# Kernel optimization log

Measured on AMD Instinct MI355X. Metric: run time of the kernel, lower is better.

## Reference

```python
import jax, jax.numpy as jnp
import numpy as np

D_MODEL = 768
HEADS = 12
D_HEAD = D_MODEL // HEADS
D_DYNA = 768
EPS = 1e-5
B, SP, SI = 16, 256, 1024


def _layernorm(x, g, b):
    mu = jnp.mean(x, axis=-1, keepdims=True)
    var = jnp.var(x, axis=-1, keepdims=True)
    return (x - mu) * jax.lax.rsqrt(var + EPS) * g + b


def _mha(q, k, v, wq, bq, wk, bk, wv, bv, wo, bo):
    # weights stored [d_in, d_out]; torch Linear math y = x @ W^T + b is
    # equivalent with transposed storage.
    B_ = q.shape[0]
    qh = (q @ wq + bq).reshape(B_, -1, HEADS, D_HEAD)
    kh = (k @ wk + bk).reshape(B_, -1, HEADS, D_HEAD)
    vh = (v @ wv + bv).reshape(B_, -1, HEADS, D_HEAD)
    scores = jnp.einsum('bqhd,bkhd->bhqk', qh, kh) / np.sqrt(D_HEAD).astype(np.float32)
    attn = jax.nn.softmax(scores, axis=-1)  # dropout disabled (eval)
    out = jnp.einsum('bhqk,bkhd->bqhd', attn, vh).reshape(B_, -1, D_MODEL)
    return out @ wo + bo


def setup_inputs() -> dict:
    key = jax.random.key(0)
    ks = iter(jax.random.split(key, 40))
    s = 0.02
    d = {
        'image': jax.random.normal(next(ks), (B, SI, D_MODEL), jnp.float32),
        'prompt': jax.random.normal(next(ks), (B, SP, D_MODEL), jnp.float32),
        'posi': jax.random.normal(next(ks), (B, SI, D_MODEL), jnp.float32),
        'posp': jax.random.normal(next(ks), (B, SP, D_MODEL), jnp.float32),
    }
    for ln in ('ln_p1', 'ln_p2', 'ln_p3', 'ln_i1'):
        d[ln + '_g'] = jnp.ones((D_MODEL,), jnp.float32)
        d[ln + '_b'] = jnp.zeros((D_MODEL,), jnp.float32)
    for pre in ('pp', 'pi'):
        for nm in ('q', 'k', 'v', 'o'):
            d[f'{pre}_w{nm}'] = s * jax.random.normal(next(ks), (D_MODEL, D_MODEL), jnp.float32)
            d[f'{pre}_b{nm}'] = jnp.zeros((D_MODEL,), jnp.float32)
    d['ff_w1'] = s * jax.random.normal(next(ks), (D_MODEL, D_MODEL), jnp.float32)
    d['ff_b1'] = jnp.zeros((D_MODEL,), jnp.float32)
    d['ff_w2'] = s * jax.random.normal(next(ks), (D_MODEL, D_DYNA), jnp.float32)
    d['ff_b2'] = jnp.zeros((D_DYNA,), jnp.float32)
    return d


def reference(image, prompt, posi, posp,
              ln_p1_g, ln_p1_b, ln_p2_g, ln_p2_b, ln_p3_g, ln_p3_b, ln_i1_g, ln_i1_b,
              pp_wq, pp_bq, pp_wk, pp_bk, pp_wv, pp_bv, pp_wo, pp_bo,
              pi_wq, pi_bq, pi_wk, pi_bk, pi_wv, pi_bv, pi_wo, pi_bo,
              ff_w1, ff_b1, ff_w2, ff_b2):
    prompt0 = prompt + posp
    xp = _layernorm(prompt0, ln_p1_g, ln_p1_b)
    xp = _mha(xp, xp, xp, pp_wq, pp_bq, pp_wk, pp_bk, pp_wv, pp_bv, pp_wo, pp_bo)
    prompt = prompt + xp  # dropout_p1 is identity in eval
    xp = _layernorm(prompt + prompt0, ln_p2_g, ln_p2_b)
    xi = _layernorm(image + posi, ln_i1_g, ln_i1_b)
    xp = _mha(xp, xi, xi, pi_wq, pi_bq, pi_wk, pi_bk, pi_wv, pi_bv, pi_wo, pi_bo)
    prompt = prompt + xp  # dropout_p2 identity
    xp = _layernorm(prompt + prompt0, ln_p3_g, ln_p3_b)
    xp = jax.nn.relu(xp @ ff_w1 + ff_b1) @ ff_w2 + ff_b2
    return xp
```

## Files before the change

kernel.cpp:

```cpp
#include <hip/hip_runtime.h>
#include <hip/hip_bf16.h>
#include <stdint.h>
#include <math.h>

#define D_MODEL 768
#define HEADS 12
#define D_HEAD 64
#define BATCH 16
#define SP 256
#define SI 1024
#define NP (BATCH * SP)
#define NI (BATCH * SI)

#define GLOBAL_AS __attribute__((address_space(1)))
#define LDS_AS    __attribute__((address_space(3)))

typedef __attribute__((ext_vector_type(8))) short  frag_ab;
typedef __attribute__((ext_vector_type(4))) float  frag_cd;

static __device__ __forceinline__ ushort f2bf(float f) {
  __hip_bfloat16 h = __float2bfloat16(f);
  return *(ushort*)&h;
}
static __device__ __forceinline__ float bf2f(ushort u) {
  return __bfloat162float(*(__hip_bfloat16*)&u);
}
static __device__ __forceinline__ bool probe_bf(const uint32_t* p) {
  return p[0] == 0x3F803F80u;
}

struct Prep {
  const void* wsrc[10]; ushort* wdst[10];
  const void* vsrc[18]; float* vdst;
};

__global__ __launch_bounds__(256) void prep_kernel(Prep p, const uint32_t* probe) {
  const bool isbf = probe_bf(probe);
  const int z = blockIdx.z;
  if (z < 10) {
    __shared__ float tile[32][33];
    const int tx = threadIdx.x & 31, ty = threadIdx.x >> 5;
    const int x0 = blockIdx.x * 32, y0 = blockIdx.y * 32;
    const void* src = p.wsrc[z];
    ushort* dst = p.wdst[z];
#pragma unroll
    for (int i = 0; i < 4; i++) {
      const int y = y0 + ty + i * 8;
      float v;
      if (isbf) v = bf2f(((const ushort*)src)[(size_t)y * 768 + x0 + tx]);
      else      v = ((const float*)src)[(size_t)y * 768 + x0 + tx];
      tile[ty + i * 8][tx] = v;
    }
    __syncthreads();
#pragma unroll
    for (int i = 0; i < 4; i++) {
      const int row = x0 + ty + i * 8;
      const int col = y0 + tx;
      dst[(size_t)row * 768 + col] = f2bf(tile[tx][ty + i * 8]);
    }
  } else {
    const int idx = (blockIdx.y * 24 + blockIdx.x) * 256 + threadIdx.x;
    if (idx < 18 * 768) {
      const int e = idx / 768, i = idx - e * 768;
      float v;
      if (isbf) v = bf2f(((const ushort*)p.vsrc[e])[i]);
      else      v = ((const float*)p.vsrc[e])[i];
      p.vdst[idx] = v;
    }
  }
}

struct LNJob {
  const void* a; const void* b;
  const float* g; const float* be;
  float* sum_out; ushort* ln_out;
  int nrows; int abf;
};

__global__ __launch_bounds__(192) void add_ln2(LNJob J0, LNJob J1, const uint32_t* probe) {
  int row = blockIdx.x;
  LNJob j = (row < J0.nrows) ? J0 : J1;
  if (row >= J0.nrows) row -= J0.nrows;
  const int tid = threadIdx.x;
  const size_t base = (size_t)row * D_MODEL;
  const int c0 = tid * 4;
  const bool isbf = j.abf && probe_bf(probe);
  float x[4];
  if (isbf) {
    const uint2 ua = *(const uint2*)((const ushort*)j.a + base + c0);
    const uint2 ub = *(const uint2*)((const ushort*)j.b + base + c0);
    const ushort* pa = (const ushort*)&ua;
    const ushort* pb = (const ushort*)&ub;
#pragma unroll
    for (int t = 0; t < 4; t++) x[t] = bf2f(pa[t]) + bf2f(pb[t]);
  } else {
    const float4 fa = *(const float4*)((const float*)j.a + base + c0);
    const float4 fb = *(const float4*)((const float*)j.b + base + c0);
    x[0] = fa.x + fb.x; x[1] = fa.y + fb.y; x[2] = fa.z + fb.z; x[3] = fa.w + fb.w;
  }
  if (j.sum_out) {
    float4 s4; s4.x = x[0]; s4.y = x[1]; s4.z = x[2]; s4.w = x[3];
    *(float4*)&j.sum_out[base + c0] = s4;
  }
  __shared__ float rs[192], rq[192];
  __shared__ float stats[2];
  rs[tid] = x[0] + x[1] + x[2] + x[3];
  rq[tid] = x[0]*x[0] + x[1]*x[1] + x[2]*x[2] + x[3]*x[3];
  __syncthreads();
  if (tid < 64) {
    float s = rs[tid] + rs[tid + 64] + rs[tid + 128];
    float q = rq[tid] + rq[tid + 64] + rq[tid + 128];
#pragma unroll
    for (int o = 32; o > 0; o >>= 1) { s += __shfl_down(s, o); q += __shfl_down(q, o); }
    if (tid == 0) {
      const float mu  = s * (1.0f / D_MODEL);
      const float var = q * (1.0f / D_MODEL) - mu * mu;
      stats[0] = mu;
      stats[1] = rsqrtf(var + 1e-5f);
    }
  }
  __syncthreads();
  const float mu = stats[0], inv = stats[1];
  const float4 gv = *(const float4*)&j.g[c0];
  const float4 bv = *(const float4*)&j.be[c0];
  uint2 ou;
  ushort* oe = (ushort*)&ou;
  oe[0] = f2bf((x[0] - mu) * inv * gv.x + bv.x);
  oe[1] = f2bf((x[1] - mu) * inv * gv.y + bv.y);
  oe[2] = f2bf((x[2] - mu) * inv * gv.z + bv.z);
  oe[3] = f2bf((x[3] - mu) * inv * gv.w + bv.w);
  *(uint2*)(j.ln_out + base + c0) = ou;
}

template<int BM>
__global__ __launch_bounds__(256) void gemm_k(
    const ushort* __restrict__ A, const ushort* __restrict__ Bt,
    const float* __restrict__ bias,
    const void* __restrict__ resid, int rmode,
    void* __restrict__ C, int relu, int omode,
    const uint32_t* __restrict__ probe, int X) {
  __shared__ ushort As[BM * 32];
  __shared__ ushort Bs[128 * 32];
  const int tid  = threadIdx.x;
  const int lane = tid & 63, w = tid >> 6;
  const int wr = w >> 1, wc = w & 1;
  const int ml = lane & 15, kq = lane >> 4;
  const int bid = blockIdx.x;
  const int rest = bid >> 3;
  const int x = rest % X, y = (bid & 7) + 8 * (rest / X);
  const int m0 = y * BM, n0 = x * 128;
  constexpr int MT   = BM / 32;
  constexpr int ASEG = BM / 16;
  constexpr int NSEG = (ASEG + 8) / 4;

  frag_cd acc[MT][4] = {};

  for (int k0 = 0; k0 < 768; k0 += 32) {
#pragma unroll
    for (int i = 0; i < NSEG; i++) {
      const int s = w + i * 4;
      const bool isA = (s < ASEG);
      const int seg = isA ? s : (s - ASEG);
      const int r   = seg * 16 + (lane >> 2);
      const int kof = k0 + (lane & 3) * 8;
      if (isA)
        __builtin_amdgcn_global_load_lds((const GLOBAL_AS void*)(A + (size_t)(m0 + r) * 768 + kof),
            (LDS_AS void*)((LDS_AS ushort*)As + seg * 512), 16, 0, 0);
      else
        __builtin_amdgcn_global_load_lds((const GLOBAL_AS void*)(Bt + (size_t)(n0 + r) * 768 + kof),
            (LDS_AS void*)((LDS_AS ushort*)Bs + seg * 512), 16, 0, 0);
    }
    __syncthreads();

    frag_ab af[MT], bf4[4];
#pragma unroll
    for (int t = 0; t < MT; t++)
      af[t] = *(const frag_ab*)&As[(wr * (BM / 2) + t * 16 + ml) * 32 + kq * 8];
#pragma unroll
    for (int t = 0; t < 4; t++)
      bf4[t] = *(const frag_ab*)&Bs[(wc * 64 + t * 16 + ml) * 32 + kq * 8];
#pragma unroll
    for (int mt = 0; mt < MT; mt++)
#pragma unroll
      for (int nt = 0; nt < 4; nt++)
        acc[mt][nt] = __builtin_amdgcn_mfma_f32_16x16x32_bf16(
            af[mt], bf4[nt], acc[mt][nt], 0, 0, 0);
    __syncthreads();
  }

  const bool obf = (omode == 1) || (omode == 2 && probe_bf(probe));
  const bool rbf = (rmode == 2) && probe_bf(probe);
#pragma unroll
  for (int mt = 0; mt < MT; mt++) {
#pragma unroll
    for (int nt = 0; nt < 4; nt++) {
      const int row0 = m0 + wr * (BM / 2) + mt * 16 + kq * 4;
      const int col  = n0 + wc * 64 + nt * 16 + ml;
      const float bc = bias[col];
#pragma unroll
      for (int r = 0; r < 4; r++) {
        const size_t off = (size_t)(row0 + r) * 768 + col;
        float v = acc[mt][nt][r] + bc;
        if (rmode != 0)
          v += rbf ? bf2f(((const ushort*)resid)[off]) : ((const float*)resid)[off];
        if (relu) v = fmaxf(v, 0.f);
        if (obf) ((ushort*)C)[off] = f2bf(v);
        else     ((float*)C)[off]  = v;
      }
    }
  }
}

struct GJob {
  const ushort* A; const ushort* Bt; const float* bias;
  ushort* o0; ushort* o1; ushort* vT;
  int X; int vsub; int shift;
};

#define BAR   __builtin_amdgcn_s_barrier()
#define LGKM0 do { asm volatile("s_waitcnt lgkmcnt(0)" ::: "memory"); \
                   __builtin_amdgcn_sched_barrier(0); } while (0)
#define VMC4  do { asm volatile("s_waitcnt vmcnt(4)" ::: "memory"); \
                   __builtin_amdgcn_sched_barrier(0); } while (0)

#define RD_A(SL) do { \
  const ushort* _b = &lds[SL][0][0]; \
  _Pragma("unroll") for (int _m = 0; _m < 4; ++_m) \
  _Pragma("unroll") for (int _k = 0; _k < 2; ++_k) \
    aF[_m][_k] = *(const frag_ab*)(_b + ((wr << 6) + _m * 16 + ml) * 64 + \
                                   (((_k << 5) + (kq << 3)) ^ swz)); \
} while (0)

#define RD_B(DST, SL, no) do { \
  const ushort* _b = &lds[SL][1][0]; \
  _Pragma("unroll") for (int _n = 0; _n < 2; ++_n) \
  _Pragma("unroll") for (int _k = 0; _k < 2; ++_k) \
    DST[_n][_k] = *(const frag_ab*)(_b + ((wc << 6) + (no) + _n * 16 + ml) * 64 + \
                                    (((_k << 5) + (kq << 3)) ^ swz)); \
} while (0)

#define MM(NB, BF) do { \
  __builtin_amdgcn_s_setprio(1); \
  _Pragma("unroll") for (int _m = 0; _m < 4; ++_m) \
  _Pragma("unroll") for (int _n = 0; _n < 2; ++_n) \
  _Pragma("unroll") for (int _k = 0; _k < 2; ++_k) \
    acc[_m][(NB) + _n] = __builtin_amdgcn_mfma_f32_16x16x32_bf16( \
        aF[_m][_k], BF[_n][_k], acc[_m][(NB) + _n], 0, 0, 0); \
  __builtin_amdgcn_s_setprio(0); \
} while (0)

#define STAGE(SL, RG, PTR, RBASE, KT) do { \
  const ushort* _p = (PTR) + (size_t)((RBASE) + srow) * 768 + ((KT) << 6) + scol; \
  _Pragma("unroll") for (int _j = 0; _j < 4; ++_j) \
    __builtin_amdgcn_global_load_lds( \
        (const GLOBAL_AS void*)(_p + (size_t)(_j * 32) * 768), \
        (LDS_AS void*)((LDS_AS ushort*)&lds[SL][RG][0] + (((_j << 2) + w) << 9)), \
        16, 0, 0); \
} while (0)

__global__ __launch_bounds__(256, 2) void gemm_mega128(GJob J0, GJob J1, int n0blocks) {
  __shared__ __align__(16) ushort lds[2][2][8192];
  int bid = blockIdx.x;
  GJob j = (bid < n0blocks) ? J0 : J1;
  if (bid >= n0blocks) bid -= n0blocks;
  const int tid  = threadIdx.x;
  const int lane = tid & 63, w = tid >> 6;
  const int wr = w >> 1, wc = w & 1;
  const int ml = lane & 15, kq = lane >> 4;
  const int rest = bid >> 3;
  const int x = rest % j.X, y = (bid & 7) + 8 * (rest / j.X);
  const int m0 = y << 7, n0 = x << 7;
  const int srow = (w << 3) + (lane >> 3);
  const int scol = (((lane & 7) ^ (lane >> 3)) << 3);
  const int swz  = (ml & 7) << 3;
  const ushort* jA = j.A;
  const ushort* jB = j.Bt;

  frag_cd acc[4][4] = {};
  frag_ab aF[4][2], bF0[2][2], bF1[2][2];

  STAGE(0, 0, jA, m0, 0);
  STAGE(0, 1, jB, n0, 0);
  STAGE(1, 0, jA, m0, 1);
  VMC4;
  BAR;

  for (int it = 0; it < 6; ++it) {
    const int t1  = 2 * it + 1;
    const int tn0 = (2 * it + 2 < 12) ? 2 * it + 2 : 11;
    const int tn1 = (2 * it + 3 < 12) ? 2 * it + 3 : 11;
    RD_A(0); RD_B(bF0, 0, 0);
    STAGE(1, 1, jB, n0, t1);
    BAR; LGKM0;
    MM(0, bF0);
    BAR;
    RD_B(bF1, 0, 32);
    STAGE(0, 0, jA, m0, tn0);
    BAR; LGKM0;
    MM(2, bF1);
    VMC4;
    BAR;
    RD_A(1); RD_B(bF0, 1, 0);
    STAGE(0, 1, jB, n0, tn0);
    BAR; LGKM0;
    MM(0, bF0);
    BAR;
    RD_B(bF1, 1, 32);
    STAGE(1, 0, jA, m0, tn1);
    BAR; LGKM0;
    MM(2, bF1);
    VMC4;
    BAR;
  }

  const int sub  = x / 6;
  const int mask = (1 << j.shift) - 1;
#pragma unroll
  for (int mt = 0; mt < 4; mt++) {
#pragma unroll
    for (int nt = 0; nt < 4; nt++) {
      const int row0 = m0 + wr * 64 + mt * 16 + kq * 4;
      const int col  = n0 + wc * 64 + nt * 16 + ml;
      const float bc = j.bias[col];
      if (sub == j.vsub) {
        const int hcol = col - sub * 768;
        const int hh = hcol >> 6, dd = hcol & 63;
        const int bb = row0 >> j.shift;
        const int jj = row0 & mask;
        uint2 pack;
        ushort* pe = (ushort*)&pack;
#pragma unroll
        for (int r = 0; r < 4; r++) pe[r] = f2bf(acc[mt][nt][r] + bc);
        *(uint2*)(j.vT + ((((size_t)(bb * HEADS + hh) << 6) + dd) << j.shift) + jj) = pack;
      } else {
        ushort* out = (sub == 0) ? j.o0 : j.o1;
        const int cl = col - sub * 768;
#pragma unroll
        for (int r = 0; r < 4; r++)
          out[(size_t)(row0 + r) * 768 + cl] = f2bf(acc[mt][nt][r] + bc);
      }
    }
  }
}

#undef RD_A
#undef RD_B
#undef MM
#undef STAGE

#define FS 68
__global__ __launch_bounds__(256) void fattn_mfma(
    const ushort* __restrict__ Q, const ushort* __restrict__ Kp,
    const ushort* __restrict__ vT, ushort* __restrict__ O, int Skv) {
  __shared__ __align__(16) ushort Qs[64 * FS];
  __shared__ __align__(16) ushort Ks[64 * FS];
  __shared__ __align__(16) ushort Vt[64 * FS];
  __shared__ __align__(16) ushort Ps[64 * FS];
  const int tid  = threadIdx.x;
  const int lane = tid & 63, w = tid >> 6;
  const int ml   = lane & 15, kq = lane >> 4;
  const int bid = blockIdx.x;
  const int g8  = bid & 7;
  const int qt  = (bid >> 3) & 3;
  const int g   = (bid >> 5) * 8 + g8;
  const int h   = g % HEADS;
  const int b   = g / HEADS;
  const int q0  = qt * 64;
  const ushort* Qb  = Q  + ((size_t)b * SP + q0) * D_MODEL + h * D_HEAD;
  const ushort* Kb  = Kp + (size_t)b * Skv * D_MODEL + h * D_HEAD;
  const ushort* vTb = vT + (size_t)g * 64 * Skv;

  for (int c = tid; c < 512; c += 256) {
    const int r = c >> 3, p = c & 7;
    *(uint4*)&Qs[r * FS + p * 8] = *(const uint4*)(Qb + (size_t)r * D_MODEL + p * 8);
  }
  __syncthreads();
  frag_ab qa[2];
#pragma unroll
  for (int kc = 0; kc < 2; kc++)
    qa[kc] = *(const frag_ab*)&Qs[(w * 16 + ml) * FS + kc * 32 + kq * 8];

  frag_cd oc[4] = {};
  float m_i[4], l_i[4];
#pragma unroll
  for (int r = 0; r < 4; r++) { m_i[r] = -1e30f; l_i[r] = 0.f; }
  const float SCL = 0.125f * 1.44269504f;

  for (int j0 = 0; j0 < Skv; j0 += 64) {
    __syncthreads();
    for (int c = tid; c < 512; c += 256) {
      const int r = c >> 3, p = c & 7;
      *(uint4*)&Ks[r * FS + p * 8] = *(const uint4*)(Kb + (size_t)(j0 + r) * D_MODEL + p * 8);
      *(uint4*)&Vt[r * FS + p * 8] = *(const uint4*)(vTb + (size_t)r * Skv + j0 + p * 8);
    }
    __syncthreads();

    frag_cd sc[4] = {};
#pragma unroll
    for (int nt = 0; nt < 4; nt++)
#pragma unroll
      for (int kc = 0; kc < 2; kc++) {
        const frag_ab bfr = *(const frag_ab*)&Ks[(nt * 16 + ml) * FS + kc * 32 + kq * 8];
        sc[nt] = __builtin_amdgcn_mfma_f32_16x16x32_bf16(qa[kc], bfr, sc[nt], 0, 0, 0);
      }
#pragma unroll
    for (int nt = 0; nt < 4; nt++)
#pragma unroll
      for (int r = 0; r < 4; r++) sc[nt][r] *= SCL;

    float al[4];
#pragma unroll
    for (int r = 0; r < 4; r++) {
      float mx = fmaxf(fmaxf(sc[0][r], sc[1][r]), fmaxf(sc[2][r], sc[3][r]));
#pragma unroll
      for (int m = 1; m < 16; m <<= 1) mx = fmaxf(mx, __shfl_xor(mx, m, 16));
      const float mnew = fmaxf(m_i[r], mx);
      al[r] = exp2f(m_i[r] - mnew);
      float p[4], s = 0.f;
#pragma unroll
      for (int nt = 0; nt < 4; nt++) { p[nt] = exp2f(sc[nt][r] - mnew); s += p[nt]; }
#pragma unroll
      for (int m = 1; m < 16; m <<= 1) s += __shfl_xor(s, m, 16);
      l_i[r] = l_i[r] * al[r] + s;
      m_i[r] = mnew;
      const int prow = (w * 16 + kq * 4 + r) * FS;
#pragma unroll
      for (int nt = 0; nt < 4; nt++) Ps[prow + nt * 16 + ml] = f2bf(p[nt]);
    }
#pragma unroll
    for (int dt = 0; dt < 4; dt++)
#pragma unroll
      for (int r = 0; r < 4; r++) oc[dt][r] *= al[r];

#pragma unroll
    for (int kc = 0; kc < 2; kc++) {
      const frag_ab pa = *(const frag_ab*)&Ps[(w * 16 + ml) * FS + kc * 32 + kq * 8];
#pragma unroll
      for (int dt = 0; dt < 4; dt++) {
        const frag_ab vb = *(const frag_ab*)&Vt[(dt * 16 + ml) * FS + kc * 32 + kq * 8];
        oc[dt] = __builtin_amdgcn_mfma_f32_16x16x32_bf16(pa, vb, oc[dt], 0, 0, 0);
      }
    }
  }

  float inv[4];
#pragma unroll
  for (int r = 0; r < 4; r++) inv[r] = 1.0f / l_i[r];
#pragma unroll
  for (int dt = 0; dt < 4; dt++)
#pragma unroll
    for (int r = 0; r < 4; r++)
      O[((size_t)b * SP + q0 + w * 16 + kq * 4 + r) * D_MODEL + h * D_HEAD + dt * 16 + ml] =
          f2bf(oc[dt][r] * inv[r]);
}

extern "C" void kernel_launch(void* const* d_in, const int* in_sizes, int n_in,
                              void* d_out, int out_size, void* d_ws, size_t ws_size,
                              hipStream_t stream) {
  (void)in_sizes; (void)n_in; (void)out_size;
  char* base = (char*)d_ws;
  size_t off = 256;
  auto alloc = [&](size_t bytes) -> char* {
    char* p = base + off;
    off = (off + bytes + 255) & ~(size_t)255;
    return p;
  };
  const size_t WB = (size_t)768 * 768 * 2;
  ushort* Wt[10];
  for (int i = 0; i < 10; i++) Wt[i] = (ushort*)alloc(WB);
  float* vecs = (float*)alloc(18 * 768 * 4);
  float* biasF[10];
  for (int i = 0; i < 10; i++) biasF[i] = vecs + i * 768;
  float* lnF = vecs + 10 * 768;
  float* prompt0 = (float*)alloc((size_t)NP * 768 * 4);
  float* cur     = (float*)alloc((size_t)NP * 768 * 4);
  ushort* q_bf   = (ushort*)alloc((size_t)NP * 768 * 2);
  ushort* k_s    = (ushort*)alloc((size_t)NP * 768 * 2);
  ushort* k_c    = (ushort*)alloc((size_t)NI * 768 * 2);
  ushort* xln_bf = (ushort*)alloc((size_t)NP * 768 * 2);
  ushort* xi_bf  = (ushort*)alloc((size_t)NI * 768 * 2);
  ushort* obuf_bf = (ushort*)alloc((size_t)NP * 768 * 2);
  ushort* ffn1_bf = (ushort*)alloc((size_t)NP * 768 * 2);
  ushort* vT_s   = (ushort*)alloc((size_t)BATCH * HEADS * 64 * SP * 2);
  ushort* vT_c   = (ushort*)alloc((size_t)BATCH * HEADS * 64 * SI * 2);
  if (ws_size < off) return;

  const uint32_t* probe = (const uint32_t*)d_in[4];
  const int widx[10] = {12, 14, 16, 18, 20, 22, 24, 26, 28, 30};
  const int bidx[10] = {13, 15, 17, 19, 21, 23, 25, 27, 29, 31};

  Prep pr{};
  for (int i = 0; i < 10; i++) { pr.wsrc[i] = d_in[widx[i]]; pr.wdst[i] = Wt[i]; }
  for (int i = 0; i < 10; i++) pr.vsrc[i] = d_in[bidx[i]];
  for (int i = 0; i < 8;  i++) pr.vsrc[10 + i] = d_in[4 + i];
  pr.vdst = vecs;
  prep_kernel<<<dim3(24, 24, 11), 256, 0, stream>>>(pr, probe);

  float* G1 = lnF + 0 * 768, *B1 = lnF + 1 * 768;
  float* G2 = lnF + 2 * 768, *B2 = lnF + 3 * 768;
  float* G3 = lnF + 4 * 768, *B3 = lnF + 5 * 768;
  float* Gi = lnF + 6 * 768, *Bi = lnF + 7 * 768;

  LNJob L0{d_in[1], d_in[3], G1, B1, prompt0, xln_bf, NP, 1};
  LNJob Li{d_in[0], d_in[2], Gi, Bi, nullptr, xi_bf,  NI, 1};
  add_ln2<<<NP + NI, 192, 0, stream>>>(L0, Li, probe);

  GJob js{xln_bf, Wt[0], biasF[0], q_bf, k_s, vT_s, 18, 2, 8};
  GJob jc{xi_bf,  Wt[5], biasF[5], k_c,  nullptr, vT_c, 12, 1, 10};
  gemm_mega128<<<576 + 1536, 256, 0, stream>>>(js, jc, 576);

  fattn_mfma<<<BATCH * HEADS * (SP / 64), 256, 0, stream>>>(q_bf, k_s, vT_s, obuf_bf, SP);

  gemm_k<64><<<6 * 64, 256, 0, stream>>>(obuf_bf, Wt[3], biasF[3],
      d_in[1], 2, cur, 0, 0, probe, 6);

  LNJob L2{cur, prompt0, G2, B2, nullptr, xln_bf, NP, 0};
  LNJob Lz{}; Lz.nrows = 0;
  add_ln2<<<NP, 192, 0, stream>>>(L2, Lz, probe);

  gemm_k<64><<<6 * 64, 256, 0, stream>>>(xln_bf, Wt[4], biasF[4],
      nullptr, 0, q_bf, 0, 1, probe, 6);

  fattn_mfma<<<BATCH * HEADS * (SP / 64), 256, 0, stream>>>(q_bf, k_c, vT_c, obuf_bf, SI);

  gemm_k<64><<<6 * 64, 256, 0, stream>>>(obuf_bf, Wt[7], biasF[7],
      cur, 1, cur, 0, 0, probe, 6);

  LNJob L3{cur, prompt0, G3, B3, nullptr, xln_bf, NP, 0};
  add_ln2<<<NP, 192, 0, stream>>>(L3, Lz, probe);

  gemm_k<64><<<6 * 64, 256, 0, stream>>>(xln_bf, Wt[8], biasF[8],
      nullptr, 0, ffn1_bf, 1, 1, probe, 6);

  gemm_k<64><<<6 * 64, 256, 0, stream>>>(ffn1_bf, Wt[9], biasF[9],
      nullptr, 0, d_out, 0, 2, probe, 6);
}
```

Measured before the change: 503.9 us.

## Use pipelined 128x128 GEMM for prompt GEMMs and prefetch K/V in attention

Replaces the simple BM=64 GEMM used for the five prompt-side projections with a new kernel built on the swizzled, double-buffered 128x128 engine already used by the fused QKV GEMM, factored into a shared macro. Flash attention now prefetches the next K/V tile into registers while computing on the current one. The goal is better MFMA utilisation and hidden global-load latency. The trade-off is fewer blocks for the 4096-row GEMMs (192 instead of 384), which may underfill the GPU's CUs.

```diff
diff --git a/kernel.cpp b/kernel.cpp
--- a/kernel.cpp
+++ b/kernel.cpp
@@ -132,91 +132,6 @@
   *(uint2*)(j.ln_out + base + c0) = ou;
 }
 
-template<int BM>
-__global__ __launch_bounds__(256) void gemm_k(
-    const ushort* __restrict__ A, const ushort* __restrict__ Bt,
-    const float* __restrict__ bias,
-    const void* __restrict__ resid, int rmode,
-    void* __restrict__ C, int relu, int omode,
-    const uint32_t* __restrict__ probe, int X) {
-  __shared__ ushort As[BM * 32];
-  __shared__ ushort Bs[128 * 32];
-  const int tid  = threadIdx.x;
-  const int lane = tid & 63, w = tid >> 6;
-  const int wr = w >> 1, wc = w & 1;
-  const int ml = lane & 15, kq = lane >> 4;
-  const int bid = blockIdx.x;
-  const int rest = bid >> 3;
-  const int x = rest % X, y = (bid & 7) + 8 * (rest / X);
-  const int m0 = y * BM, n0 = x * 128;
-  constexpr int MT   = BM / 32;
-  constexpr int ASEG = BM / 16;
-  constexpr int NSEG = (ASEG + 8) / 4;
-
-  frag_cd acc[MT][4] = {};
-
-  for (int k0 = 0; k0 < 768; k0 += 32) {
-#pragma unroll
-    for (int i = 0; i < NSEG; i++) {
-      const int s = w + i * 4;
-      const bool isA = (s < ASEG);
-      const int seg = isA ? s : (s - ASEG);
-      const int r   = seg * 16 + (lane >> 2);
-      const int kof = k0 + (lane & 3) * 8;
-      if (isA)
-        __builtin_amdgcn_global_load_lds((const GLOBAL_AS void*)(A + (size_t)(m0 + r) * 768 + kof),
-            (LDS_AS void*)((LDS_AS ushort*)As + seg * 512), 16, 0, 0);
-      else
-        __builtin_amdgcn_global_load_lds((const GLOBAL_AS void*)(Bt + (size_t)(n0 + r) * 768 + kof),
-            (LDS_AS void*)((LDS_AS ushort*)Bs + seg * 512), 16, 0, 0);
-    }
-    __syncthreads();
-
-    frag_ab af[MT], bf4[4];
-#pragma unroll
-    for (int t = 0; t < MT; t++)
-      af[t] = *(const frag_ab*)&As[(wr * (BM / 2) + t * 16 + ml) * 32 + kq * 8];
-#pragma unroll
-    for (int t = 0; t < 4; t++)
-      bf4[t] = *(const frag_ab*)&Bs[(wc * 64 + t * 16 + ml) * 32 + kq * 8];
-#pragma unroll
-    for (int mt = 0; mt < MT; mt++)
-#pragma unroll
-      for (int nt = 0; nt < 4; nt++)
-        acc[mt][nt] = __builtin_amdgcn_mfma_f32_16x16x32_bf16(
-            af[mt], bf4[nt], acc[mt][nt], 0, 0, 0);
-    __syncthreads();
-  }
-
-  const bool obf = (omode == 1) || (omode == 2 && probe_bf(probe));
-  const bool rbf = (rmode == 2) && probe_bf(probe);
-#pragma unroll
-  for (int mt = 0; mt < MT; mt++) {
-#pragma unroll
-    for (int nt = 0; nt < 4; nt++) {
-      const int row0 = m0 + wr * (BM / 2) + mt * 16 + kq * 4;
-      const int col  = n0 + wc * 64 + nt * 16 + ml;
-      const float bc = bias[col];
-#pragma unroll
-      for (int r = 0; r < 4; r++) {
-        const size_t off = (size_t)(row0 + r) * 768 + col;
-        float v = acc[mt][nt][r] + bc;
-        if (rmode != 0)
-          v += rbf ? bf2f(((const ushort*)resid)[off]) : ((const float*)resid)[off];
-        if (relu) v = fmaxf(v, 0.f);
-        if (obf) ((ushort*)C)[off] = f2bf(v);
-        else     ((float*)C)[off]  = v;
-      }
-    }
-  }
-}
-
-struct GJob {
-  const ushort* A; const ushort* Bt; const float* bias;
-  ushort* o0; ushort* o1; ushort* vT;
-  int X; int vsub; int shift;
-};
-
 #define BAR   __builtin_amdgcn_s_barrier()
 #define LGKM0 do { asm volatile("s_waitcnt lgkmcnt(0)" ::: "memory"); \
                    __builtin_amdgcn_sched_barrier(0); } while (0)
@@ -257,6 +172,44 @@
         (LDS_AS void*)((LDS_AS ushort*)&lds[SL][RG][0] + (((_j << 2) + w) << 9)), \
         16, 0, 0); \
 } while (0)
+
+#define ENGINE128() do { \
+  STAGE(0, 0, jA, m0, 0); \
+  STAGE(0, 1, jB, n0, 0); \
+  STAGE(1, 0, jA, m0, 1); \
+  VMC4; BAR; \
+  for (int it = 0; it < 6; ++it) { \
+    const int t1  = 2 * it + 1; \
+    const int tn0 = (2 * it + 2 < 12) ? 2 * it + 2 : 11; \
+    const int tn1 = (2 * it + 3 < 12) ? 2 * it + 3 : 11; \
+    RD_A(0); RD_B(bF0, 0, 0); \
+    STAGE(1, 1, jB, n0, t1); \
+    BAR; LGKM0; \
+    MM(0, bF0); \
+    BAR; \
+    RD_B(bF1, 0, 32); \
+    STAGE(0, 0, jA, m0, tn0); \
+    BAR; LGKM0; \
+    MM(2, bF1); \
+    VMC4; BAR; \
+    RD_A(1); RD_B(bF0, 1, 0); \
+    STAGE(0, 1, jB, n0, tn0); \
+    BAR; LGKM0; \
+    MM(0, bF0); \
+    BAR; \
+    RD_B(bF1, 1, 32); \
+    STAGE(1, 0, jA, m0, tn1); \
+    BAR; LGKM0; \
+    MM(2, bF1); \
+    VMC4; BAR; \
+  } \
+} while (0)
+
+struct GJob {
+  const ushort* A; const ushort* Bt; const float* bias;
+  ushort* o0; ushort* o1; ushort* vT;
+  int X; int vsub; int shift;
+};
 
 __global__ __launch_bounds__(256, 2) void gemm_mega128(GJob J0, GJob J1, int n0blocks) {
   __shared__ __align__(16) ushort lds[2][2][8192];
@@ -279,39 +232,7 @@
   frag_cd acc[4][4] = {};
   frag_ab aF[4][2], bF0[2][2], bF1[2][2];
 
-  STAGE(0, 0, jA, m0, 0);
-  STAGE(0, 1, jB, n0, 0);
-  STAGE(1, 0, jA, m0, 1);
-  VMC4;
-  BAR;
-
-  for (int it = 0; it < 6; ++it) {
-    const int t1  = 2 * it + 1;
-    const int tn0 = (2 * it + 2 < 12) ? 2 * it + 2 : 11;
-    const int tn1 = (2 * it + 3 < 12) ? 2 * it + 3 : 11;
-    RD_A(0); RD_B(bF0, 0, 0);
-    STAGE(1, 1, jB, n0, t1);
-    BAR; LGKM0;
-    MM(0, bF0);
-    BAR;
-    RD_B(bF1, 0, 32);
-    STAGE(0, 0, jA, m0, tn0);
-    BAR; LGKM0;
-    MM(2, bF1);
-    VMC4;
-    BAR;
-    RD_A(1); RD_B(bF0, 1, 0);
-    STAGE(0, 1, jB, n0, tn0);
-    BAR; LGKM0;
-    MM(0, bF0);
-    BAR;
-    RD_B(bF1, 1, 32);
-    STAGE(1, 0, jA, m0, tn1);
-    BAR; LGKM0;
-    MM(2, bF1);
-    VMC4;
-    BAR;
-  }
+  ENGINE128();
 
   const int sub  = x / 6;
   const int mask = (1 << j.shift) - 1;
@@ -343,10 +264,60 @@
   }
 }
 
+__global__ __launch_bounds__(256, 2) void gemm_v3(
+    const ushort* __restrict__ A, const ushort* __restrict__ Bt,
+    const float* __restrict__ bias,
+    const void* __restrict__ resid, int rmode,
+    void* __restrict__ C, int relu, int omode,
+    const uint32_t* __restrict__ probe, int X) {
+  __shared__ __align__(16) ushort lds[2][2][8192];
+  const int bid = blockIdx.x;
+  const int tid  = threadIdx.x;
+  const int lane = tid & 63, w = tid >> 6;
+  const int wr = w >> 1, wc = w & 1;
+  const int ml = lane & 15, kq = lane >> 4;
+  const int rest = bid >> 3;
+  const int x = rest % X, y = (bid & 7) + 8 * (rest / X);
+  const int m0 = y << 7, n0 = x << 7;
+  const int srow = (w << 3) + (lane >> 3);
+  const int scol = (((lane & 7) ^ (lane >> 3)) << 3);
+  const int swz  = (ml & 7) << 3;
+  const ushort* jA = A;
+  const ushort* jB = Bt;
+
+  frag_cd acc[4][4] = {};
+  frag_ab aF[4][2], bF0[2][2], bF1[2][2];
+
+  ENGINE128();
+
+  const bool obf = (omode == 1) || (omode == 2 && probe_bf(probe));
+  const bool rbf = (rmode == 2) && probe_bf(probe);
+#pragma unroll
+  for (int mt = 0; mt < 4; mt++) {
+#pragma unroll
+    for (int nt = 0; nt < 4; nt++) {
+      const int row0 = m0 + wr * 64 + mt * 16 + kq * 4;
+      const int col  = n0 + wc * 64 + nt * 16 + ml;
+      const float bc = bias[col];
+#pragma unroll
+      for (int r = 0; r < 4; r++) {
+        const size_t off = (size_t)(row0 + r) * 768 + col;
+        float v = acc[mt][nt][r] + bc;
+        if (rmode != 0)
+          v += rbf ? bf2f(((const ushort*)resid)[off]) : ((const float*)resid)[off];
+        if (relu) v = fmaxf(v, 0.f);
+        if (obf) ((ushort*)C)[off] = f2bf(v);
+        else     ((float*)C)[off]  = v;
+      }
+    }
+  }
+}
+
 #undef RD_A
 #undef RD_B
 #undef MM
 #undef STAGE
+#undef ENGINE128
 
 #define FS 68
 __global__ __launch_bounds__(256) void fattn_mfma(
@@ -370,6 +341,9 @@
   const ushort* Kb  = Kp + (size_t)b * Skv * D_MODEL + h * D_HEAD;
   const ushort* vTb = vT + (size_t)g * 64 * Skv;
 
+  const int r0 = tid >> 3, p0 = tid & 7;
+  const int r1 = r0 + 32;
+
   for (int c = tid; c < 512; c += 256) {
     const int r = c >> 3, p = c & 7;
     *(uint4*)&Qs[r * FS + p * 8] = *(const uint4*)(Qb + (size_t)r * D_MODEL + p * 8);
@@ -386,14 +360,25 @@
   for (int r = 0; r < 4; r++) { m_i[r] = -1e30f; l_i[r] = 0.f; }
   const float SCL = 0.125f * 1.44269504f;
 
+  uint4 kr0 = *(const uint4*)(Kb + (size_t)r0 * D_MODEL + p0 * 8);
+  uint4 vr0 = *(const uint4*)(vTb + (size_t)r0 * Skv + p0 * 8);
+  uint4 kr1 = *(const uint4*)(Kb + (size_t)r1 * D_MODEL + p0 * 8);
+  uint4 vr1 = *(const uint4*)(vTb + (size_t)r1 * Skv + p0 * 8);
+
   for (int j0 = 0; j0 < Skv; j0 += 64) {
     __syncthreads();
-    for (int c = tid; c < 512; c += 256) {
-      const int r = c >> 3, p = c & 7;
-      *(uint4*)&Ks[r * FS + p * 8] = *(const uint4*)(Kb + (size_t)(j0 + r) * D_MODEL + p * 8);
-      *(uint4*)&Vt[r * FS + p * 8] = *(const uint4*)(vTb + (size_t)r * Skv + j0 + p * 8);
-    }
+    *(uint4*)&Ks[r0 * FS + p0 * 8] = kr0;
+    *(uint4*)&Vt[r0 * FS + p0 * 8] = vr0;
+    *(uint4*)&Ks[r1 * FS + p0 * 8] = kr1;
+    *(uint4*)&Vt[r1 * FS + p0 * 8] = vr1;
     __syncthreads();
+    if (j0 + 64 < Skv) {
+      const int jn = j0 + 64;
+      kr0 = *(const uint4*)(Kb + (size_t)(jn + r0) * D_MODEL + p0 * 8);
+      vr0 = *(const uint4*)(vTb + (size_t)r0 * Skv + jn + p0 * 8);
+      kr1 = *(const uint4*)(Kb + (size_t)(jn + r1) * D_MODEL + p0 * 8);
+      vr1 = *(const uint4*)(vTb + (size_t)r1 * Skv + jn + p0 * 8);
+    }
 
     frag_cd sc[4] = {};
 #pragma unroll
@@ -511,27 +496,27 @@
 
   fattn_mfma<<<BATCH * HEADS * (SP / 64), 256, 0, stream>>>(q_bf, k_s, vT_s, obuf_bf, SP);
 
-  gemm_k<64><<<6 * 64, 256, 0, stream>>>(obuf_bf, Wt[3], biasF[3],
+  gemm_v3<<<192, 256, 0, stream>>>(obuf_bf, Wt[3], biasF[3],
       d_in[1], 2, cur, 0, 0, probe, 6);
 
   LNJob L2{cur, prompt0, G2, B2, nullptr, xln_bf, NP, 0};
   LNJob Lz{}; Lz.nrows = 0;
   add_ln2<<<NP, 192, 0, stream>>>(L2, Lz, probe);
 
-  gemm_k<64><<<6 * 64, 256, 0, stream>>>(xln_bf, Wt[4], biasF[4],
+  gemm_v3<<<192, 256, 0, stream>>>(xln_bf, Wt[4], biasF[4],
       nullptr, 0, q_bf, 0, 1, probe, 6);
 
   fattn_mfma<<<BATCH * HEADS * (SP / 64), 256, 0, stream>>>(q_bf, k_c, vT_c, obuf_bf, SI);
 
-  gemm_k<64><<<6 * 64, 256, 0, stream>>>(obuf_bf, Wt[7], biasF[7],
+  gemm_v3<<<192, 256, 0, stream>>>(obuf_bf, Wt[7], biasF[7],
       cur, 1, cur, 0, 0, probe, 6);
 
   LNJob L3{cur, prompt0, G3, B3, nullptr, xln_bf, NP, 0};
   add_ln2<<<NP, 192, 0, stream>>>(L3, Lz, probe);
 
-  gemm_k<64><<<6 * 64, 256, 0, stream>>>(xln_bf, Wt[8], biasF[8],
+  gemm_v3<<<192, 256, 0, stream>>>(xln_bf, Wt[8], biasF[8],
       nullptr, 0, ffn1_bf, 1, 1, probe, 6);
 
-  gemm_k<64><<<6 * 64, 256, 0, stream>>>(ffn1_bf, Wt[9], biasF[9],
+  gemm_v3<<<192, 256, 0, stream>>>(ffn1_bf, Wt[9], biasF[9],
       nullptr, 0, d_out, 0, 2, probe, 6);
 }
```

Result: no change. 497.8 us (-1.2%).
